# Kernel tuning notes

Hardware: AMD Instinct MI355X
Metric: run time of the kernel (lower is better)

The kernel has to match this reference:

```python
import jax, jax.numpy as jnp
import numpy as np

EMBED = 512
HEADS = 64
DK = EMBED // HEADS  # == n_wires_attn == 8
NW_FFN = 8
FFN = 2048
EPS = 1e-5


def _layernorm(x, g, b):
    mu = jnp.mean(x, axis=-1, keepdims=True)
    var = jnp.var(x, axis=-1, keepdims=True)
    return (x - mu) * jax.lax.rsqrt(var + EPS) * g + b


def setup_inputs() -> dict:
    key = jax.random.key(0)
    ks = jax.random.split(key, 12)
    d = {
        "x": jax.random.normal(ks[0], (4, 1024, EMBED), dtype=jnp.float32),
        # attention quantum RX params (one per wire, shared across heads/tokens)
        "phi": jax.random.normal(ks[1], (DK,), dtype=jnp.float32) * 0.1,
        # combine_heads linear
        "Wc": jax.random.normal(ks[2], (EMBED, EMBED), dtype=jnp.float32) / np.sqrt(EMBED),
        "bc": jnp.zeros((EMBED,), dtype=jnp.float32),
        # FFN quantum RY params
        "theta": jax.random.normal(ks[3], (NW_FFN,), dtype=jnp.float32) * 0.1,
        "W1": jax.random.normal(ks[4], (NW_FFN, FFN), dtype=jnp.float32) / np.sqrt(NW_FFN),
        "b1": jnp.zeros((FFN,), dtype=jnp.float32),
        "W2": jax.random.normal(ks[5], (FFN, EMBED), dtype=jnp.float32) / np.sqrt(FFN),
        "b2": jnp.zeros((EMBED,), dtype=jnp.float32),
        "g1": jnp.ones((EMBED,), dtype=jnp.float32),
        "be1": jnp.zeros((EMBED,), dtype=jnp.float32),
        "g2": jnp.ones((EMBED,), dtype=jnp.float32),
        "be2": jnp.zeros((EMBED,), dtype=jnp.float32),
    }
    return d


def reference(x, phi, Wc, bc, theta, W1, b1, W2, b2, g1, be1, g2, be2):
    B, S, E = x.shape
    # --- quantum attention projections ---
    # Per head-row of DK features: RX(x_i) encoder then trainable RX(phi_i),
    xh = x.reshape(B, S, HEADS, DK)
    qkv = jnp.cos(xh + phi)                     # [B,S,H,DK]
    qkv = jnp.transpose(qkv, (0, 2, 1, 3))      # [B,H,S,DK]
    scores = jnp.einsum('bhqd,bhkd->bhqk', qkv, qkv) / jnp.sqrt(jnp.float32(DK))
    attn = jax.nn.softmax(scores, axis=-1)
    out = jnp.einsum('bhqk,bhkd->bhqd', attn, qkv)
    out = jnp.transpose(out, (0, 2, 1, 3)).reshape(B, S, E)
    attn_out = out @ Wc.T if False else out @ Wc + bc  # combine_heads linear
    x1 = _layernorm(x + attn_out, g1, be1)
    # --- quantum FFN: RX(x_i) then trainable RY(theta_i) -> <Z> = cos(x_i)*cos(theta_i)
    qout = jnp.cos(x1[..., :NW_FFN]) * jnp.cos(theta)   # [B,S,NW_FFN]
    h = jax.nn.relu(qout @ W1 + b1)
    ffn_out = h @ W2 + b2
    return _layernorm(x1 + ffn_out, g2, be2)
```

## Files before the change

kernel.cpp:

```cpp
#include <hip/hip_runtime.h>
#include <hip/hip_bf16.h>
#include <math.h>

#define B 4
#define S 1024
#define E 512
#define H 64
#define DK 8
#define FFN 2048
#define BS (B*S)

#define CSCALE 0.7141879f

#if __has_builtin(__builtin_amdgcn_exp2f)
#define EXP2F(x) __builtin_amdgcn_exp2f(x)
#else
#define EXP2F(x) exp2f(x)
#endif

typedef __attribute__((ext_vector_type(8))) short short8;
typedef __attribute__((ext_vector_type(4))) float float4a;

union U8 { short8 v; unsigned u[4]; };
union F4 { float4a v; float f[4]; };

__device__ __forceinline__ unsigned short f2bf(float f) {
    unsigned u = __builtin_bit_cast(unsigned, f);
    u = (u + 0x7fffu + ((u >> 16) & 1u)) >> 16;
    return (unsigned short)u;
}
__device__ __forceinline__ float bf2f(unsigned short h) {
    return __builtin_bit_cast(float, (unsigned)h << 16);
}
__device__ __forceinline__ unsigned packbf(float a, float b) {
    return __builtin_amdgcn_perm(__builtin_bit_cast(unsigned, a),
                                 __builtin_bit_cast(unsigned, b), 0x07060302u);
}
__device__ __forceinline__ unsigned packbf_rn(float a, float b) {
    return ((unsigned)f2bf(a) << 16) | f2bf(b);
}
__device__ __forceinline__ int pidx(int k) {
    return (k & ~31) | (((k >> 2) & 3) << 3) | (((k >> 4) & 1) << 2) | (k & 3);
}

__device__ __forceinline__ void glds16(const void* g, void* l) {
    __builtin_amdgcn_global_load_lds(
        (const __attribute__((address_space(1))) void*)g,
        (__attribute__((address_space(3))) void*)l, 16, 0, 0);
}

__global__ __launch_bounds__(512) void attn_conv_kernel(const float* __restrict__ x,
                                                        const float* __restrict__ phi,
                                                        const float* __restrict__ Wc,
                                                        const float* __restrict__ W2,
                                                        const float* __restrict__ W1,
                                                        const float* __restrict__ b1,
                                                        unsigned short* __restrict__ Afrag,
                                                        unsigned short* __restrict__ W2f,
                                                        unsigned short* __restrict__ Wcf,
                                                        unsigned short* __restrict__ W1f) {
    __shared__ unsigned short kv[(S + 16) * DK];
    __shared__ unsigned short vtp[9][S + 8];
    int bid = blockIdx.x;
    int tid = threadIdx.x;
    const short8 z8 = {0,0,0,0,0,0,0,0};

    if (bid < 336) {
        int idx = bid * 512 + tid;
        if (idx < 131072) {
            int lane = idx & 63, c = idx >> 6;
            int ntile = c >> 6, kb32 = c & 63;
            int g = lane >> 4, col = lane & 15;
            int n = ntile * 16 + col, kb = kb32 * 32;
            short8 o;
            #pragma unroll
            for (int j = 0; j < 8; j++) {
                int k = kb + 16 * (j >> 2) + 4 * g + (j & 3);
                o[j] = (short)f2bf(W2[(size_t)k * 512 + n]);
            }
            *(short8*)&W2f[(size_t)idx * 8] = o;
        } else if (idx < 163840) {
            int i2 = idx - 131072;
            int lane = i2 & 63, c = i2 >> 6;
            int ntile = c >> 4, kb32 = c & 15;
            int g = lane >> 4, col = lane & 15;
            int n = ntile * 16 + col, kb = kb32 * 32;
            short8 o;
            #pragma unroll
            for (int j = 0; j < 8; j++)
                o[j] = (short)f2bf(Wc[(size_t)(kb + g * 8 + j) * 512 + n]);
            *(short8*)&Wcf[(size_t)i2 * 8] = o;
        } else {
            int i3 = idx - 163840;
            if (i3 < 4096) {
                int f = i3 >> 1, gg = i3 & 1;
                short8 o = z8;
                if (gg == 0) {
                    #pragma unroll
                    for (int j = 0; j < 8; j++) o[j] = (short)f2bf(W1[j * FFN + f]);
                } else {
                    o[0] = (short)f2bf(b1[f]);
                }
                *(short8*)&W1f[(size_t)i3 * 8] = o;
            }
        }
        return;
    }

    int abid = bid - 336;
    int head = abid >> 2, qquad = abid & 3;
    int b = head >> 6, hh = head & 63;

    float ph[DK];
    #pragma unroll
    for (int d = 0; d < DK; d++) ph[d] = phi[d];

    {
        int r2 = tid * 2;
        unsigned short vb[8][2];
        #pragma unroll
        for (int j = 0; j < 2; j++) {
            const float* xp = x + ((size_t)(b * S + r2 + j)) * E + hh * DK;
            float4 u = *(const float4*)xp;
            float4 v = *(const float4*)(xp + 4);
            float c[8] = {__cosf(u.x+ph[0]), __cosf(u.y+ph[1]), __cosf(u.z+ph[2]), __cosf(u.w+ph[3]),
                          __cosf(v.x+ph[4]), __cosf(v.y+ph[5]), __cosf(v.z+ph[6]), __cosf(v.w+ph[7])};
            U8 kr;
            kr.u[0] = packbf_rn(c[1] * CSCALE, c[0] * CSCALE);
            kr.u[1] = packbf_rn(c[3] * CSCALE, c[2] * CSCALE);
            kr.u[2] = packbf_rn(c[5] * CSCALE, c[4] * CSCALE);
            kr.u[3] = packbf_rn(c[7] * CSCALE, c[6] * CSCALE);
            *(short8*)&kv[(r2 + j) * DK] = kr.v;
            #pragma unroll
            for (int d = 0; d < 8; d++) vb[d][j] = f2bf(c[d]);
        }
        int pr = pidx(r2);
        #pragma unroll
        for (int d = 0; d < 8; d++)
            *(unsigned*)&vtp[d][pr] = (unsigned)vb[d][0] | ((unsigned)vb[d][1] << 16);
        *(unsigned*)&vtp[8][pr] = 0x3F803F80u;
    }
    if (tid < 16) *(short8*)&kv[(S + tid) * DK] = z8;
    __syncthreads();

    int w = tid >> 6, lane = tid & 63, col = lane & 15, g = lane >> 4;
    bool g0 = (g == 0);
    int q0 = qquad * 256 + w * 32;
    const float4a zc = {0.f,0.f,0.f,0.f};

    short8 aq[2];
    #pragma unroll
    for (int t = 0; t < 2; t++)
        aq[t] = g0 ? *(const short8*)&kv[(q0 + t*16 + col) * DK] : z8;

    float4a acc[2];
    acc[0] = zc; acc[1] = zc;

    int vrow = col < 8 ? col : 8;
    const unsigned short* vbase = &vtp[vrow][0];

    int off0 = g0 ? col * DK : S * DK;
    int off1 = g0 ? (16 + col) * DK : S * DK;
    int stepo = g0 ? 32 * DK : 0;

    for (int kb = 0; kb < S; kb += 32) {
        short8 bk0 = *(const short8*)&kv[off0];
        short8 bk1 = *(const short8*)&kv[off1];
        off0 += stepo; off1 += stepo;
        short8 vf = *(const short8*)(vbase + kb + g * 8);
        #pragma unroll
        for (int t = 0; t < 2; t++) {
            float4a s0 = __builtin_amdgcn_mfma_f32_16x16x32_bf16(bk0, aq[t], zc, 0,0,0);
            float4a s1 = __builtin_amdgcn_mfma_f32_16x16x32_bf16(bk1, aq[t], zc, 0,0,0);
            F4 S0, S1; S0.v = s0; S1.v = s1;
            float e00 = EXP2F(S0.f[0]);
            float e01 = EXP2F(S0.f[1]);
            float e02 = EXP2F(S0.f[2]);
            float e03 = EXP2F(S0.f[3]);
            float e10 = EXP2F(S1.f[0]);
            float e11 = EXP2F(S1.f[1]);
            float e12 = EXP2F(S1.f[2]);
            float e13 = EXP2F(S1.f[3]);
            U8 pf;
            pf.u[0] = packbf(e01, e00);
            pf.u[1] = packbf(e03, e02);
            pf.u[2] = packbf(e11, e10);
            pf.u[3] = packbf(e13, e12);
            acc[t] = __builtin_amdgcn_mfma_f32_16x16x32_bf16(vf, pf.v, acc[t], 0,0,0);
        }
    }
    int lp8 = ((hh & 3) * 16 + col) * 8;
    #pragma unroll
    for (int t = 0; t < 2; t++) {
        F4 a; a.v = acc[t];
        float denom = __shfl(a.f[0], 32 + col);
        float inv = __builtin_amdgcn_rcpf(denom);
        if (g < 2) {
            int chunk = (hh >> 2) * 256 + (b * 64 + qquad * 16 + w * 2 + t);
            uint2 o;
            o.x = packbf_rn(a.f[1] * inv, a.f[0] * inv);
            o.y = packbf_rn(a.f[3] * inv, a.f[2] * inv);
            *(uint2*)&Afrag[(size_t)chunk * 512 + lp8 + g * 4] = o;
        }
    }
}

__global__ __launch_bounds__(512) void combine_ln1(const unsigned short* __restrict__ Afrag,
                                                   const unsigned short* __restrict__ Wcf,
                                                   const float* __restrict__ bc,
                                                   const float* __restrict__ x,
                                                   const float* __restrict__ g1,
                                                   const float* __restrict__ be1,
                                                   float* __restrict__ x1out,
                                                   unsigned short* __restrict__ qoutbf,
                                                   const float* __restrict__ theta) {
    __shared__ unsigned short As[16 * 64 * 8];
    __shared__ unsigned short Wcs[2][2048 * 8];
    __shared__ float xout[16][516];
    int tt = blockIdx.x;
    int tid = threadIdx.x;
    int w = tid >> 6, lane = tid & 63;
    int wbase = (tid & ~63) * 8;

    #pragma unroll
    for (int r = 0; r < 2; r++) {
        const unsigned short* gsrc =
            Afrag + ((size_t)((r * 8 + w) * 256 + tt) * 64 + lane) * 8;
        glds16(gsrc, &As[r * 4096 + wbase]);
    }
    #pragma unroll
    for (int r = 0; r < 4; r++) {
        int nt = r * 8 + w;
        glds16(Wcf + ((size_t)(nt * 16 + 0) * 64 + lane) * 8, &Wcs[0][nt * 512]);
    }
    #pragma unroll
    for (int r = 0; r < 4; r++) {
        int nt = r * 8 + w;
        glds16(Wcf + ((size_t)(nt * 16 + 1) * 64 + lane) * 8, &Wcs[1][nt * 512]);
    }
    asm volatile("s_waitcnt vmcnt(4)" ::: "memory");
    __builtin_amdgcn_s_barrier();

    int col = lane & 15, g = lane >> 4;
    const float4a zc = {0.f,0.f,0.f,0.f};
    float4a acc[4];
    #pragma unroll
    for (int nt = 0; nt < 4; nt++) acc[nt] = zc;

    for (int kb32 = 0; kb32 < 16; kb32++) {
        int cur = kb32 & 1;
        short8 af = *(const short8*)&As[(kb32 * 64 + lane) * 8];
        #pragma unroll
        for (int nt = 0; nt < 4; nt++) {
            short8 bf = *(const short8*)&Wcs[cur][((w * 4 + nt) * 64 + lane) * 8];
            acc[nt] = __builtin_amdgcn_mfma_f32_16x16x32_bf16(af, bf, acc[nt], 0, 0, 0);
        }
        if (kb32 < 15) {
            asm volatile("s_waitcnt lgkmcnt(0)" ::: "memory");
            __builtin_amdgcn_s_barrier();
            if (kb32 < 14) {
                #pragma unroll
                for (int r = 0; r < 4; r++) {
                    int nt = r * 8 + w;
                    glds16(Wcf + ((size_t)(nt * 16 + kb32 + 2) * 64 + lane) * 8,
                           &Wcs[cur][nt * 512]);
                }
                asm volatile("s_waitcnt vmcnt(4)" ::: "memory");
            } else {
                asm volatile("s_waitcnt vmcnt(0)" ::: "memory");
            }
            __builtin_amdgcn_s_barrier();
        }
    }
    #pragma unroll
    for (int nt = 0; nt < 4; nt++) {
        int n = w * 64 + nt * 16 + col;
        float bb = bc[n];
        #pragma unroll
        for (int r = 0; r < 4; r++)
            xout[g * 4 + r][n] = acc[nt][r] + bb;
    }
    __syncthreads();

    int hl = lane >> 5, l = lane & 31;
    int token = w * 2 + hl;
    int e0 = l * 16;
    size_t grow = ((size_t)tt * 16 + token) * 512;
    float v[16];
    float s = 0.f, sq = 0.f;
    #pragma unroll
    for (int u = 0; u < 4; u++) {
        float4 xv = *(const float4*)&x[grow + e0 + u * 4];
        float4 pv = *(const float4*)&xout[token][e0 + u * 4];
        float a0 = xv.x + pv.x, a1 = xv.y + pv.y, a2 = xv.z + pv.z, a3 = xv.w + pv.w;
        v[u*4] = a0; v[u*4+1] = a1; v[u*4+2] = a2; v[u*4+3] = a3;
        s += a0 + a1 + a2 + a3;
        sq += a0*a0 + a1*a1 + a2*a2 + a3*a3;
    }
    #pragma unroll
    for (int off = 1; off <= 16; off <<= 1) {
        s  += __shfl_xor(s, off);
        sq += __shfl_xor(sq, off);
    }
    float mu = s * (1.f / 512.f);
    float var = sq * (1.f / 512.f) - mu * mu;
    float rstd = rsqrtf(var + 1e-5f);
    float y[16];
    #pragma unroll
    for (int u = 0; u < 4; u++) {
        float4 gv = *(const float4*)&g1[e0 + u * 4];
        float4 bv = *(const float4*)&be1[e0 + u * 4];
        y[u*4]   = (v[u*4]   - mu) * rstd * gv.x + bv.x;
        y[u*4+1] = (v[u*4+1] - mu) * rstd * gv.y + bv.y;
        y[u*4+2] = (v[u*4+2] - mu) * rstd * gv.z + bv.z;
        y[u*4+3] = (v[u*4+3] - mu) * rstd * gv.w + bv.w;
        float4 o = make_float4(y[u*4], y[u*4+1], y[u*4+2], y[u*4+3]);
        *(float4*)&x1out[grow + e0 + u * 4] = o;
    }
    if (l == 0) {
        U8 q;
        q.u[0] = packbf_rn(__cosf(y[1]) * __cosf(theta[1]), __cosf(y[0]) * __cosf(theta[0]));
        q.u[1] = packbf_rn(__cosf(y[3]) * __cosf(theta[3]), __cosf(y[2]) * __cosf(theta[2]));
        q.u[2] = packbf_rn(__cosf(y[5]) * __cosf(theta[5]), __cosf(y[4]) * __cosf(theta[4]));
        q.u[3] = packbf_rn(__cosf(y[7]) * __cosf(theta[7]), __cosf(y[6]) * __cosf(theta[6]));
        *(short8*)&qoutbf[((size_t)tt * 16 + token) * 8] = q.v;
    }
}

__global__ __launch_bounds__(256) void ffn_mfma(const unsigned short* __restrict__ qbf,
                                                const unsigned short* __restrict__ W1fg,
                                                const unsigned short* __restrict__ W2f,
                                                const float* __restrict__ b2,
                                                unsigned short* __restrict__ Cbf) {
    __shared__ unsigned short w1x[FFN * 16];
    int tid = threadIdx.x;
    int wbase = (tid & ~63) * 8;
    #pragma unroll
    for (int r = 0; r < 16; r++)
        glds16(W1fg + (size_t)(r * 256 + tid) * 8, &w1x[r * 2048 + wbase]);
    asm volatile("s_waitcnt vmcnt(0)" ::: "memory");
    __syncthreads();

    int w = tid >> 6, lane = tid & 63, col = lane & 15, g = lane >> 4;
    int tb = blockIdx.x >> 2, nb = blockIdx.x & 3;
    int tg = w >> 1, ngw = w & 1;
    int mw = tb * 64 + tg * 32;
    int ntile0 = nb * 8 + ngw * 4;
    const short8 z8 = {0,0,0,0,0,0,0,0};
    const short8 one8 = {(short)0x3F80,0,0,0,0,0,0,0};
    const float4a zc = {0.f,0.f,0.f,0.f};

    short8 qf[2];
    #pragma unroll
    for (int t = 0; t < 2; t++)
        qf[t] = (g == 0) ? *(const short8*)&qbf[(size_t)(mw + t * 16 + col) * 8]
                         : (g == 1 ? one8 : z8);

    float4a acc[2][4];
    #pragma unroll
    for (int t = 0; t < 2; t++)
        #pragma unroll
        for (int nt = 0; nt < 4; nt++) acc[t][nt] = zc;

    const unsigned short* w2p = W2f + (size_t)ntile0 * 64 * 512 + lane * 8;

    short8 afA[4], afB[4];
    #pragma unroll
    for (int nt = 0; nt < 4; nt++)
        afA[nt] = *(const short8*)(w2p + nt * 32768);

#define FFN_BODY(KB32, AF)                                                        \
    {                                                                             \
        int kb = (KB32) * 32;                                                     \
        short8 w1f0 = (g < 2) ? *(const short8*)&w1x[(kb + col) * 16 + g * 8] : z8;      \
        short8 w1f1 = (g < 2) ? *(const short8*)&w1x[(kb + 16 + col) * 16 + g * 8] : z8; \
        _Pragma("unroll")                                                         \
        for (int t = 0; t < 2; t++) {                                             \
            float4a h0 = __builtin_amdgcn_mfma_f32_16x16x32_bf16(w1f0, qf[t], zc, 0,0,0); \
            float4a h1 = __builtin_amdgcn_mfma_f32_16x16x32_bf16(w1f1, qf[t], zc, 0,0,0); \
            F4 H0, H1; H0.v = h0; H1.v = h1;                                      \
            float e00 = fmaxf(H0.f[0], 0.f);                                      \
            float e01 = fmaxf(H0.f[1], 0.f);                                      \
            float e02 = fmaxf(H0.f[2], 0.f);                                      \
            float e03 = fmaxf(H0.f[3], 0.f);                                      \
            float e10 = fmaxf(H1.f[0], 0.f);                                      \
            float e11 = fmaxf(H1.f[1], 0.f);                                      \
            float e12 = fmaxf(H1.f[2], 0.f);                                      \
            float e13 = fmaxf(H1.f[3], 0.f);                                      \
            U8 pf;                                                                \
            pf.u[0] = packbf(e01, e00);                                           \
            pf.u[1] = packbf(e03, e02);                                           \
            pf.u[2] = packbf(e11, e10);                                           \
            pf.u[3] = packbf(e13, e12);                                           \
            _Pragma("unroll")                                                     \
            for (int nt = 0; nt < 4; nt++)                                        \
                acc[t][nt] = __builtin_amdgcn_mfma_f32_16x16x32_bf16(AF[nt], pf.v, \
                                                                     acc[t][nt], 0,0,0); \
        }                                                                         \
    }

    for (int kb32 = 0; kb32 < 64; kb32 += 2) {
        #pragma unroll
        for (int nt = 0; nt < 4; nt++)
            afB[nt] = *(const short8*)(w2p + nt * 32768 + (kb32 + 1) * 512);
        FFN_BODY(kb32, afA)
        if (kb32 + 2 < 64) {
            #pragma unroll
            for (int nt = 0; nt < 4; nt++)
                afA[nt] = *(const short8*)(w2p + nt * 32768 + (kb32 + 2) * 512);
        }
        FFN_BODY(kb32 + 1, afB)
    }
#undef FFN_BODY

    int n0 = ntile0 * 16;
    #pragma unroll
    for (int nt = 0; nt < 4; nt++) {
        float4 bb = *(const float4*)&b2[n0 + nt * 16 + 4 * g];
        #pragma unroll
        for (int t = 0; t < 2; t++) {
            F4 a; a.v = acc[t][nt];
            uint2 o;
            o.x = packbf_rn(a.f[1] + bb.y, a.f[0] + bb.x);
            o.y = packbf_rn(a.f[3] + bb.w, a.f[2] + bb.z);
            *(uint2*)&Cbf[(size_t)(mw + t * 16 + col) * 512 + n0 + nt * 16 + 4 * g] = o;
        }
    }
}

__global__ __launch_bounds__(256) void ln_kernel(const float* __restrict__ a,
                                                 const unsigned short* __restrict__ r,
                                                 const float* __restrict__ g,
                                                 const float* __restrict__ be,
                                                 float* __restrict__ out) {
    int t = blockIdx.x * 4 + (threadIdx.x >> 6);
    int lane = threadIdx.x & 63;
    size_t base = (size_t)t * E;
    int e0 = lane * 8;
    float4 a0 = *(const float4*)&a[base + e0];
    float4 a1 = *(const float4*)&a[base + e0 + 4];
    uint4 rv = *(const uint4*)&r[base + e0];
    float v[8];
    v[0] = a0.x + bf2f((unsigned short)(rv.x & 0xffff));
    v[1] = a0.y + bf2f((unsigned short)(rv.x >> 16));
    v[2] = a0.z + bf2f((unsigned short)(rv.y & 0xffff));
    v[3] = a0.w + bf2f((unsigned short)(rv.y >> 16));
    v[4] = a1.x + bf2f((unsigned short)(rv.z & 0xffff));
    v[5] = a1.y + bf2f((unsigned short)(rv.z >> 16));
    v[6] = a1.z + bf2f((unsigned short)(rv.w & 0xffff));
    v[7] = a1.w + bf2f((unsigned short)(rv.w >> 16));
    float s = 0.f, sq = 0.f;
    #pragma unroll
    for (int i = 0; i < 8; i++) { s += v[i]; sq += v[i] * v[i]; }
    #pragma unroll
    for (int off = 1; off <= 32; off <<= 1) {
        s  += __shfl_xor(s, off);
        sq += __shfl_xor(sq, off);
    }
    float mu = s * (1.f / E);
    float var = sq * (1.f / E) - mu * mu;
    float rstd = rsqrtf(var + 1e-5f);
    float4 g0 = *(const float4*)&g[e0];
    float4 g1v = *(const float4*)&g[e0 + 4];
    float4 b0 = *(const float4*)&be[e0];
    float4 b1v = *(const float4*)&be[e0 + 4];
    float4 o0, o1;
    o0.x = (v[0] - mu) * rstd * g0.x + b0.x;
    o0.y = (v[1] - mu) * rstd * g0.y + b0.y;
    o0.z = (v[2] - mu) * rstd * g0.z + b0.z;
    o0.w = (v[3] - mu) * rstd * g0.w + b0.w;
    o1.x = (v[4] - mu) * rstd * g1v.x + b1v.x;
    o1.y = (v[5] - mu) * rstd * g1v.y + b1v.y;
    o1.z = (v[6] - mu) * rstd * g1v.z + b1v.z;
    o1.w = (v[7] - mu) * rstd * g1v.w + b1v.w;
    *(float4*)&out[base + e0] = o0;
    *(float4*)&out[base + e0 + 4] = o1;
}

extern "C" void kernel_launch(void* const* d_in, const int* in_sizes, int n_in,
                              void* d_out, int out_size, void* d_ws, size_t ws_size,
                              hipStream_t stream) {
    const float* x     = (const float*)d_in[0];
    const float* phi   = (const float*)d_in[1];
    const float* Wc    = (const float*)d_in[2];
    const float* bc    = (const float*)d_in[3];
    const float* theta = (const float*)d_in[4];
    const float* W1    = (const float*)d_in[5];
    const float* b1    = (const float*)d_in[6];
    const float* W2    = (const float*)d_in[7];
    const float* b2    = (const float*)d_in[8];
    const float* g1    = (const float*)d_in[9];
    const float* be1   = (const float*)d_in[10];
    const float* g2    = (const float*)d_in[11];
    const float* be2   = (const float*)d_in[12];
    float* out = (float*)d_out;

    float* ws = (float*)d_ws;
    unsigned short* Afrag  = (unsigned short*)ws;
    unsigned short* W2f    = (unsigned short*)(ws + 1048576);
    unsigned short* Wcf    = (unsigned short*)(ws + 1572864);
    unsigned short* W1f    = (unsigned short*)(ws + 1703936);
    unsigned short* qoutbf = (unsigned short*)(ws + 1736704);

    attn_conv_kernel<<<1360, 512, 0, stream>>>(x, phi, Wc, W2, W1, b1,
                                               Afrag, W2f, Wcf, W1f);
    combine_ln1<<<256, 512, 0, stream>>>(Afrag, Wcf, bc, x, g1, be1,
                                         out, qoutbf, theta);
    ffn_mfma<<<256, 256, 0, stream>>>(qoutbf, W1f, W2f, b2, Afrag);
    ln_kernel<<<1024, 256, 0, stream>>>(out, Afrag, g2, be2, out);
}
```

Before: 164.1 us.

## Split FFN reduction across waves, compact W1 layout, software-pipeline attention loop

The FFN kernel now splits its 2048-wide hidden dimension across two wave pairs and reduces the partial accumulators through shared memory. The grid doubles to 512 blocks, each covering 32 tokens instead of 64. W1 is stored compactly, with bias in a separate array, which halves the LDS staging footprint. The attention loop prefetches the next K fragments, issues all four score MFMAs up front, and raises wave priority around the MFMAs to overlap exp work with matrix ops. In exchange it adds a block-level sync, extra LDS traffic for the reduction, and doubles the W1 staging work per token.

```diff
diff --git a/kernel.cpp b/kernel.cpp
--- a/kernel.cpp
+++ b/kernel.cpp
@@ -92,16 +92,14 @@
             *(short8*)&Wcf[(size_t)i2 * 8] = o;
         } else {
             int i3 = idx - 163840;
-            if (i3 < 4096) {
-                int f = i3 >> 1, gg = i3 & 1;
-                short8 o = z8;
-                if (gg == 0) {
-                    #pragma unroll
-                    for (int j = 0; j < 8; j++) o[j] = (short)f2bf(W1[j * FFN + f]);
-                } else {
-                    o[0] = (short)f2bf(b1[f]);
-                }
+            if (i3 < 2048) {
+                short8 o;
+                #pragma unroll
+                for (int j = 0; j < 8; j++) o[j] = (short)f2bf(W1[j * FFN + i3]);
                 *(short8*)&W1f[(size_t)i3 * 8] = o;
+            } else if (i3 < 4096) {
+                int f = i3 - 2048;
+                W1f[16384 + f] = f2bf(b1[f]);
             }
         }
         return;
@@ -163,31 +161,53 @@
     int off1 = g0 ? (16 + col) * DK : S * DK;
     int stepo = g0 ? 32 * DK : 0;
 
+    short8 bk0 = *(const short8*)&kv[off0];
+    short8 bk1 = *(const short8*)&kv[off1];
+    off0 += stepo; off1 += stepo;
+
     for (int kb = 0; kb < S; kb += 32) {
-        short8 bk0 = *(const short8*)&kv[off0];
-        short8 bk1 = *(const short8*)&kv[off1];
+        __builtin_amdgcn_s_setprio(1);
+        float4a s00 = __builtin_amdgcn_mfma_f32_16x16x32_bf16(bk0, aq[0], zc, 0,0,0);
+        float4a s01 = __builtin_amdgcn_mfma_f32_16x16x32_bf16(bk1, aq[0], zc, 0,0,0);
+        float4a s10 = __builtin_amdgcn_mfma_f32_16x16x32_bf16(bk0, aq[1], zc, 0,0,0);
+        float4a s11 = __builtin_amdgcn_mfma_f32_16x16x32_bf16(bk1, aq[1], zc, 0,0,0);
+        __builtin_amdgcn_s_setprio(0);
+        short8 vf = *(const short8*)(vbase + kb + g * 8);
+        short8 nbk0 = *(const short8*)&kv[off0];
+        short8 nbk1 = *(const short8*)&kv[off1];
         off0 += stepo; off1 += stepo;
-        short8 vf = *(const short8*)(vbase + kb + g * 8);
-        #pragma unroll
-        for (int t = 0; t < 2; t++) {
-            float4a s0 = __builtin_amdgcn_mfma_f32_16x16x32_bf16(bk0, aq[t], zc, 0,0,0);
-            float4a s1 = __builtin_amdgcn_mfma_f32_16x16x32_bf16(bk1, aq[t], zc, 0,0,0);
-            F4 S0, S1; S0.v = s0; S1.v = s1;
-            float e00 = EXP2F(S0.f[0]);
-            float e01 = EXP2F(S0.f[1]);
-            float e02 = EXP2F(S0.f[2]);
-            float e03 = EXP2F(S0.f[3]);
-            float e10 = EXP2F(S1.f[0]);
-            float e11 = EXP2F(S1.f[1]);
-            float e12 = EXP2F(S1.f[2]);
-            float e13 = EXP2F(S1.f[3]);
-            U8 pf;
-            pf.u[0] = packbf(e01, e00);
-            pf.u[1] = packbf(e03, e02);
-            pf.u[2] = packbf(e11, e10);
-            pf.u[3] = packbf(e13, e12);
-            acc[t] = __builtin_amdgcn_mfma_f32_16x16x32_bf16(vf, pf.v, acc[t], 0,0,0);
-        }
+        F4 S00, S01, S10, S11;
+        S00.v = s00; S01.v = s01; S10.v = s10; S11.v = s11;
+        float ea0 = EXP2F(S00.f[0]);
+        float ea1 = EXP2F(S00.f[1]);
+        float ea2 = EXP2F(S00.f[2]);
+        float ea3 = EXP2F(S00.f[3]);
+        float eb0 = EXP2F(S01.f[0]);
+        float eb1 = EXP2F(S01.f[1]);
+        float eb2 = EXP2F(S01.f[2]);
+        float eb3 = EXP2F(S01.f[3]);
+        float ec0 = EXP2F(S10.f[0]);
+        float ec1 = EXP2F(S10.f[1]);
+        float ec2 = EXP2F(S10.f[2]);
+        float ec3 = EXP2F(S10.f[3]);
+        float ed0 = EXP2F(S11.f[0]);
+        float ed1 = EXP2F(S11.f[1]);
+        float ed2 = EXP2F(S11.f[2]);
+        float ed3 = EXP2F(S11.f[3]);
+        U8 pf0, pf1;
+        pf0.u[0] = packbf(ea1, ea0);
+        pf0.u[1] = packbf(ea3, ea2);
+        pf0.u[2] = packbf(eb1, eb0);
+        pf0.u[3] = packbf(eb3, eb2);
+        pf1.u[0] = packbf(ec1, ec0);
+        pf1.u[1] = packbf(ec3, ec2);
+        pf1.u[2] = packbf(ed1, ed0);
+        pf1.u[3] = packbf(ed3, ed2);
+        __builtin_amdgcn_s_setprio(1);
+        acc[0] = __builtin_amdgcn_mfma_f32_16x16x32_bf16(vf, pf0.v, acc[0], 0,0,0);
+        acc[1] = __builtin_amdgcn_mfma_f32_16x16x32_bf16(vf, pf1.v, acc[1], 0,0,0);
+        __builtin_amdgcn_s_setprio(0);
+        bk0 = nbk0; bk1 = nbk1;
     }
     int lp8 = ((hh & 3) * 16 + col) * 8;
     #pragma unroll
@@ -332,20 +352,24 @@
                                                 const unsigned short* __restrict__ W2f,
                                                 const float* __restrict__ b2,
                                                 unsigned short* __restrict__ Cbf) {
-    __shared__ unsigned short w1x[FFN * 16];
+    __shared__ unsigned short w1x[FFN * 8];
+    __shared__ unsigned short b1s[FFN];
+    __shared__ float accs[2][64][36];
     int tid = threadIdx.x;
     int wbase = (tid & ~63) * 8;
     #pragma unroll
-    for (int r = 0; r < 16; r++)
+    for (int r = 0; r < 8; r++)
         glds16(W1fg + (size_t)(r * 256 + tid) * 8, &w1x[r * 2048 + wbase]);
+    glds16(W1fg + 16384 + (size_t)tid * 8, &b1s[wbase]);
     asm volatile("s_waitcnt vmcnt(0)" ::: "memory");
     __syncthreads();
 
     int w = tid >> 6, lane = tid & 63, col = lane & 15, g = lane >> 4;
+    int ngw = w & 1, kh = w >> 1;
     int tb = blockIdx.x >> 2, nb = blockIdx.x & 3;
-    int tg = w >> 1, ngw = w & 1;
-    int mw = tb * 64 + tg * 32;
+    int mw = tb * 32;
     int ntile0 = nb * 8 + ngw * 4;
+    int kb32b = kh * 32;
     const short8 z8 = {0,0,0,0,0,0,0,0};
     const short8 one8 = {(short)0x3F80,0,0,0,0,0,0,0};
     const float4a zc = {0.f,0.f,0.f,0.f};
@@ -367,13 +391,20 @@
     short8 afA[4], afB[4];
     #pragma unroll
     for (int nt = 0; nt < 4; nt++)
-        afA[nt] = *(const short8*)(w2p + nt * 32768);
+        afA[nt] = *(const short8*)(w2p + nt * 32768 + (size_t)kb32b * 512);
 
 #define FFN_BODY(KB32, AF)                                                        \
     {                                                                             \
         int kb = (KB32) * 32;                                                     \
-        short8 w1f0 = (g < 2) ? *(const short8*)&w1x[(kb + col) * 16 + g * 8] : z8;      \
-        short8 w1f1 = (g < 2) ? *(const short8*)&w1x[(kb + 16 + col) * 16 + g * 8] : z8; \
+        short8 w1f0, w1f1;                                                        \
+        if (g == 0) {                                                             \
+            w1f0 = *(const short8*)&w1x[(kb + col) * 8];                          \
+            w1f1 = *(const short8*)&w1x[(kb + 16 + col) * 8];                     \
+        } else if (g == 1) {                                                      \
+            w1f0 = z8; w1f1 = z8;                                                 \
+            w1f0[0] = (short)b1s[kb + col];                                       \
+            w1f1[0] = (short)b1s[kb + 16 + col];                                  \
+        } else { w1f0 = z8; w1f1 = z8; }                                          \
         _Pragma("unroll")                                                         \
         for (int t = 0; t < 2; t++) {                                             \
             float4a h0 = __builtin_amdgcn_mfma_f32_16x16x32_bf16(w1f0, qf[t], zc, 0,0,0); \
@@ -399,31 +430,48 @@
         }                                                                         \
     }
 
-    for (int kb32 = 0; kb32 < 64; kb32 += 2) {
+    for (int i = 0; i < 32; i += 2) {
+        int kb32 = kb32b + i;
         #pragma unroll
         for (int nt = 0; nt < 4; nt++)
-            afB[nt] = *(const short8*)(w2p + nt * 32768 + (kb32 + 1) * 512);
+            afB[nt] = *(const short8*)(w2p + nt * 32768 + (size_t)(kb32 + 1) * 512);
         FFN_BODY(kb32, afA)
-        if (kb32 + 2 < 64) {
+        if (i + 2 < 32) {
             #pragma unroll
             for (int nt = 0; nt < 4; nt++)
-                afA[nt] = *(const short8*)(w2p + nt * 32768 + (kb32 + 2) * 512);
+                afA[nt] = *(const short8*)(w2p + nt * 32768 + (size_t)(kb32 + 2) * 512);
         }
         FFN_BODY(kb32 + 1, afB)
     }
 #undef FFN_BODY
 
-    int n0 = ntile0 * 16;
-    #pragma unroll
-    for (int nt = 0; nt < 4; nt++) {
-        float4 bb = *(const float4*)&b2[n0 + nt * 16 + 4 * g];
-        #pragma unroll
-        for (int t = 0; t < 2; t++) {
-            F4 a; a.v = acc[t][nt];
-            uint2 o;
-            o.x = packbf_rn(a.f[1] + bb.y, a.f[0] + bb.x);
-            o.y = packbf_rn(a.f[3] + bb.w, a.f[2] + bb.z);
-            *(uint2*)&Cbf[(size_t)(mw + t * 16 + col) * 512 + n0 + nt * 16 + 4 * g] = o;
+    if (kh == 1) {
+        #pragma unroll
+        for (int t = 0; t < 2; t++)
+            #pragma unroll
+            for (int nt = 0; nt < 4; nt++)
+                *(float4a*)&accs[ngw][lane][(t * 4 + nt) * 4] = acc[t][nt];
+    }
+    __syncthreads();
+    if (kh == 0) {
+        #pragma unroll
+        for (int t = 0; t < 2; t++)
+            #pragma unroll
+            for (int nt = 0; nt < 4; nt++)
+                acc[t][nt] = acc[t][nt] +
+                    *(const float4a*)&accs[ngw][lane][(t * 4 + nt) * 4];
+        int n0 = ntile0 * 16;
+        #pragma unroll
+        for (int nt = 0; nt < 4; nt++) {
+            float4 bb = *(const float4*)&b2[n0 + nt * 16 + 4 * g];
+            #pragma unroll
+            for (int t = 0; t < 2; t++) {
+                F4 a; a.v = acc[t][nt];
+                uint2 o;
+                o.x = packbf_rn(a.f[1] + bb.y, a.f[0] + bb.x);
+                o.y = packbf_rn(a.f[3] + bb.w, a.f[2] + bb.z);
+                *(uint2*)&Cbf[(size_t)(mw + t * 16 + col) * 512 + n0 + nt * 16 + 4 * g] = o;
+            }
         }
     }
 }
@@ -506,6 +554,6 @@
                                                Afrag, W2f, Wcf, W1f);
     combine_ln1<<<256, 512, 0, stream>>>(Afrag, Wcf, bc, x, g1, be1,
                                          out, qoutbf, theta);
-    ffn_mfma<<<256, 256, 0, stream>>>(qoutbf, W1f, W2f, b2, Afrag);
+    ffn_mfma<<<512, 256, 0, stream>>>(qoutbf, W1f, W2f, b2, Afrag);
     ln_kernel<<<1024, 256, 0, stream>>>(out, Afrag, g2, be2, out);
 }
```

After: 158.6 us. 3.3% less time.
